# Kernel tuning notes

Measured on AMD Instinct MI355X. Metric: run time of the kernel, lower is better.

Reference implementation:

```python
import jax, jax.numpy as jnp
import numpy as np
from jax import lax

B, S, H = 4, 4096, 1024
P, D = 4096, 512
K = 3                      # conv kernel size
DILATIONS = (1, 2, 4)
TOP_K = 2
INTER = min(1024, P)       # AttentionRouter.intermediate_dim
DIV_SCALE = 0.01
LN_EPS = 1e-5


def setup_inputs() -> dict:
    key = jax.random.key(0)
    ks = jax.random.split(key, 24)
    sd = 0.02
    inp = {
        "x": jax.random.normal(ks[0], (B, S, H), jnp.float32),
        "tensor_pool": jax.random.normal(ks[1], (P, D), jnp.float32),
        # router MLP
        "w1": jax.random.normal(ks[2], (INTER, H), jnp.float32) * sd,
        "b1": jnp.zeros((INTER,), jnp.float32),
        "w2": jax.random.normal(ks[3], (P, INTER), jnp.float32) * sd,
        "b2": jnp.zeros((P,), jnp.float32),
        "temperature": jnp.float32(0.5),
        # input projection + layernorm
        "wproj": jax.random.normal(ks[4], (D, H), jnp.float32) * sd,
        "bproj": jnp.zeros((D,), jnp.float32),
        "ln_g": jnp.ones((D,), jnp.float32),
        "ln_b": jnp.zeros((D,), jnp.float32),
        # mapping linear (2D -> D)
        "wmap": jax.random.normal(ks[5], (D, 2 * D), jnp.float32) * sd,
        "bmap": jnp.zeros((D,), jnp.float32),
        # dilated convs: [n_dil, out=H, in=H, K]
        "conv_w": jax.random.normal(ks[6], (len(DILATIONS), H, H, K), jnp.float32) * sd,
        "conv_b": jnp.zeros((len(DILATIONS), H), jnp.float32),
        # conv out_proj (3H -> H)
        "wout": jax.random.normal(ks[7], (H, H * len(DILATIONS)), jnp.float32) * sd,
        "bout": jnp.zeros((H,), jnp.float32),
        # router_proj (D -> H)
        "wrp": jax.random.normal(ks[8], (H, D), jnp.float32) * sd,
        "brp": jnp.zeros((H,), jnp.float32),
        # gate_proj (H -> 1)
        "wg": jax.random.normal(ks[9], (1, H), jnp.float32) * sd,
        "bg": jnp.zeros((1,), jnp.float32),
    }
    return inp


def _layernorm(x, g, b):
    mu = jnp.mean(x, axis=-1, keepdims=True)
    var = jnp.mean(jnp.square(x - mu), axis=-1, keepdims=True)
    return (x - mu) * lax.rsqrt(var + LN_EPS) * g + b


def _forward(x, tensor_pool, w1, b1, w2, b2, temperature, wproj, bproj, ln_g, ln_b,
             wmap, bmap, conv_w, conv_b, wout, bout, wrp, brp, wg, bg):
    # ---- local branch: dilated hierarchical convolution ----
    xt = jnp.transpose(x, (0, 2, 1))  # [B,H,S]
    conv_outs = []
    for i, dil in enumerate(DILATIONS):
        pad = (K - 1) // 2 * dil
        o = lax.conv_general_dilated(
            xt, conv_w[i], window_strides=(1,), padding=[(pad, pad)],
            rhs_dilation=(dil,), dimension_numbers=("NCH", "OIH", "NCH"))
        o = o + conv_b[i][None, :, None]
        o = jax.nn.gelu(o, approximate=False)  # torch nn.GELU default (erf)
        conv_outs.append(jnp.transpose(o, (0, 2, 1)))  # [B,S,H]
    concat_out = jnp.concatenate(conv_outs, axis=-1)    # [B,S,3H]
    local_out = concat_out @ wout.T + bout               # [B,S,H]

    # ---- router (global branch) ----
    inter = jax.nn.relu(x @ w1.T + b1)                   # [B,S,INTER]
    logits = inter @ w2.T + b2                           # [B,S,P]
    temp = jnp.clip(temperature, 0.1, 5.0)
    scaled = jnp.clip(logits / temp, -10.0, 10.0)
    topk_vals, topk_idx = lax.top_k(scaled, TOP_K)       # [B,S,k]
    topk_w = jax.nn.softmax(topk_vals, axis=-1)          # [B,S,k]
    experts = tensor_pool[topk_idx]                      # [B,S,k,D] gather
    weighted_map = jnp.einsum("bsk,bskd->bsd", topk_w, experts)
    projected_x = _layernorm(x @ wproj.T + bproj, ln_g, ln_b)  # [B,S,D]
    combined = jnp.concatenate([projected_x, weighted_map], axis=-1)
    transformation = combined @ wmap.T + bmap            # [B,S,D]

    # diversity loss
    usage = jnp.zeros((P,), x.dtype).at[topk_idx.reshape(-1)].add(topk_w.reshape(-1))
    frac = usage / (usage.sum() + 1e-8)
    scale = min(1.0, (B * S * H) / (P * TOP_K))
    div_loss = jnp.mean(jnp.square(frac - 1.0 / P)) * scale * DIV_SCALE

    global_out = transformation @ wrp.T + brp            # [B,S,H]
    gate = jax.nn.sigmoid(x @ wg.T + bg)                 # [B,S,1]
    attn_out = gate * local_out + (1.0 - gate) * global_out
    return attn_out, div_loss


def reference(x, tensor_pool, w1, b1, w2, b2, temperature, wproj, bproj, ln_g, ln_b,
              wmap, bmap, conv_w, conv_b, wout, bout, wrp, brp, wg, bg):
    return _forward(x, tensor_pool, w1, b1, w2, b2, temperature, wproj, bproj,
                    ln_g, ln_b, wmap, bmap, conv_w, conv_b, wout, bout,
                    wrp, brp, wg, bg)
```

## Files before the change

### kernel.cpp

```cpp
#include <hip/hip_runtime.h>
#include <math.h>
#include <climits>

#define SQ 4096
#define HD 1024
#define PD 4096
#define DD 512
#define MR 16384
#define INTERD 1024
#define SP 4104
#define NCAND 6

typedef __attribute__((ext_vector_type(8))) short short8;
typedef __attribute__((ext_vector_type(4))) float f32x4;

__device__ __forceinline__ unsigned short f2bf(float f) {
    union { float f; unsigned u; } v; v.f = f;
    unsigned r = v.u + 0x7fff + ((v.u >> 16) & 1);
    return (unsigned short)(r >> 16);
}

__device__ __forceinline__ void gll16(const unsigned short* g, unsigned short* l) {
    __builtin_amdgcn_global_load_lds(
        (const __attribute__((address_space(1))) void*)g,
        (__attribute__((address_space(3))) void*)l, 16, 0, 0);
}

template<int AMODE, int BMODE, int EPI>
__global__ __launch_bounds__(256)
void bgemm_k(const unsigned short* __restrict__ A, int lda,
             const unsigned short* __restrict__ Bm, int ldb,
             const float* __restrict__ bias,
             float* __restrict__ Cf, unsigned short* __restrict__ Cb,
             int ldc, int coff, int K, int dil,
             const float* __restrict__ gate,
             float* __restrict__ cand_v, int* __restrict__ cand_i)
{
    __shared__ __align__(16) unsigned short As[128 * 64];
    __shared__ __align__(16) unsigned short Bs[128 * 64];
    const int tid = threadIdx.x;
    const int w = tid >> 6;
    const int ln = tid & 63;
    const int bm = blockIdx.y * 128;
    const int bn = blockIdx.x * 128;
    const int wm = (w >> 1) * 64;
    const int wn = (w & 1) * 64;

    f32x4 acc[4][4] = {};

    const int l8 = (ln & 7) * 8;
    const int rsub = w * 8 + (ln >> 3);

    for (int kt = 0; kt < K; kt += 64) {
        const int tap = kt >> 10;
        const int cin0 = kt & 1023;
#pragma unroll
        for (int q = 0; q < 4; ++q) {
            const int r = q * 32 + rsub;
            const unsigned short* asrc;
            if (AMODE == 0) {
                asrc = A + (size_t)(bm + r) * lda + kt + l8;
            } else {
                int m = bm + r;
                int b = m >> 12;
                int s = m & (SQ - 1);
                asrc = A + (size_t)(b * SP + s + 4 + (tap - 1) * dil) * 1024 + cin0 + l8;
            }
            gll16(asrc, &As[q * 2048 + w * 512]);
            const unsigned short* bsrc;
            if (BMODE == 0) {
                bsrc = Bm + (size_t)(bn + r) * ldb + kt + l8;
            } else {
                bsrc = Bm + (size_t)(tap * 1024 + bn + r) * 1024 + cin0 + l8;
            }
            gll16(bsrc, &Bs[q * 2048 + w * 512]);
        }
        __syncthreads();
#pragma unroll
        for (int ks = 0; ks < 2; ++ks) {
            const int kb = ks * 32 + (ln >> 4) * 8;
            short8 af[4], bf[4];
#pragma unroll
            for (int i = 0; i < 4; ++i)
                af[i] = *(const short8*)&As[(wm + i * 16 + (ln & 15)) * 64 + kb];
#pragma unroll
            for (int j = 0; j < 4; ++j)
                bf[j] = *(const short8*)&Bs[(wn + j * 16 + (ln & 15)) * 64 + kb];
#pragma unroll
            for (int i = 0; i < 4; ++i)
#pragma unroll
                for (int j = 0; j < 4; ++j)
                    acc[i][j] = __builtin_amdgcn_mfma_f32_16x16x32_bf16(
                        af[i], bf[j], acc[i][j], 0, 0, 0);
        }
        __syncthreads();
    }

    if constexpr (EPI == 4) {
        const int g = blockIdx.x * 2 + (w & 1);
#pragma unroll
        for (int i = 0; i < 4; ++i) {
#pragma unroll
            for (int r = 0; r < 4; ++r) {
                float v0 = -1e30f, v1 = -1e30f; int i0 = INT_MAX, i1 = INT_MAX;
#pragma unroll
                for (int j = 0; j < 4; ++j) {
                    const int col = bn + wn + j * 16 + (ln & 15);
                    float v = acc[i][j][r] + bias[col];
                    if (v > v0 || (v == v0 && col < i0)) { v1 = v0; i1 = i0; v0 = v; i0 = col; }
                    else if (v > v1 || (v == v1 && col < i1)) { v1 = v; i1 = col; }
                }
#pragma unroll
                for (int msk = 1; msk <= 8; msk <<= 1) {
                    float ov0 = __shfl_xor(v0, msk); int oi0 = __shfl_xor(i0, msk);
                    float ov1 = __shfl_xor(v1, msk); int oi1 = __shfl_xor(i1, msk);
                    if (ov0 > v0 || (ov0 == v0 && oi0 < i0)) {
                        if (v0 > ov1 || (v0 == ov1 && i0 < oi1)) { v1 = v0; i1 = i0; }
                        else { v1 = ov1; i1 = oi1; }
                        v0 = ov0; i0 = oi0;
                    } else {
                        if (ov0 > v1 || (ov0 == v1 && oi0 < i1)) { v1 = ov0; i1 = oi0; }
                    }
                }
                if ((ln & 15) == 0) {
                    const int row = bm + wm + i * 16 + (ln >> 4) * 4 + r;
                    size_t base = (size_t)row * 128 + g * 2;
                    cand_v[base] = v0; cand_v[base + 1] = v1;
                    cand_i[base] = i0; cand_i[base + 1] = i1;
                }
            }
        }
        return;
    }

#pragma unroll
    for (int i = 0; i < 4; ++i) {
        const int mrow = bm + wm + i * 16 + (ln >> 4) * 4;
#pragma unroll
        for (int j = 0; j < 4; ++j) {
            const int ncol = bn + wn + j * 16 + (ln & 15);
            const float bs = bias[ncol];
#pragma unroll
            for (int r = 0; r < 4; ++r) {
                const int m = mrow + r;
                float v = acc[i][j][r] + bs;
                if (EPI == 0) {
                    Cf[(size_t)m * ldc + coff + ncol] = v;
                } else if (EPI == 1) {
                    v = 0.5f * v * (1.0f + erff(v * 0.70710678118654752f));
                    Cb[(size_t)m * ldc + coff + ncol] = f2bf(v);
                } else if (EPI == 2) {
                    Cb[(size_t)m * ldc + coff + ncol] = f2bf(v);
                } else if (EPI == 3) {
                    float g = gate[m];
                    size_t o = (size_t)m * 1024 + ncol;
                    Cf[o] = g * v + (1.0f - g) * Cf[o];
                }
            }
        }
    }
}

__global__ __launch_bounds__(256)
void gemm_relu_k(const float* __restrict__ A, const float* __restrict__ Bm,
                 const float* __restrict__ bias,
                 float* __restrict__ C, unsigned short* __restrict__ Cb)
{
    __shared__ float As[16][68];
    __shared__ float Bs[16][68];
    const int tid = threadIdx.x;
    const int tx = tid & 15;
    const int ty = tid >> 4;
    const int bm = blockIdx.y * 64;
    const int bn = blockIdx.x * 64;

    float acc[4][4];
#pragma unroll
    for (int i = 0; i < 4; ++i)
#pragma unroll
        for (int j = 0; j < 4; ++j) acc[i][j] = 0.f;

    for (int kt = 0; kt < HD; kt += 16) {
#pragma unroll
        for (int l = 0; l < 4; ++l) {
            int idx = tid + l * 256;
            int r = idx >> 4;
            int c = idx & 15;
            As[c][r] = A[(size_t)(bm + r) * HD + (kt + c)];
            Bs[c][r] = Bm[(size_t)(bn + r) * HD + (kt + c)];
        }
        __syncthreads();
#pragma unroll
        for (int c = 0; c < 16; ++c) {
            float a[4], b[4];
#pragma unroll
            for (int i = 0; i < 4; ++i) a[i] = As[c][ty * 4 + i];
#pragma unroll
            for (int j = 0; j < 4; ++j) b[j] = Bs[c][tx * 4 + j];
#pragma unroll
            for (int i = 0; i < 4; ++i)
#pragma unroll
                for (int j = 0; j < 4; ++j)
                    acc[i][j] = fmaf(a[i], b[j], acc[i][j]);
        }
        __syncthreads();
    }
#pragma unroll
    for (int i = 0; i < 4; ++i)
#pragma unroll
        for (int j = 0; j < 4; ++j) {
            int n = bn + tx * 4 + j;
            size_t o = (size_t)(bm + ty * 4 + i) * INTERD + n;
            float v = fmaxf(acc[i][j] + bias[n], 0.f);
            C[o] = v;
            Cb[o] = f2bf(v);
        }
}

__global__ __launch_bounds__(128)
void rescore_k(const float* __restrict__ cand_v, const int* __restrict__ cand_i,
               const float* __restrict__ inter, const float* __restrict__ w2,
               const float* __restrict__ b2, const float* __restrict__ tptr,
               const float* __restrict__ pool,
               unsigned short* __restrict__ combined_b, float* __restrict__ usage)
{
    const int row = blockIdx.x;
    const int t = threadIdx.x;
    __shared__ float xs[1024];
    __shared__ float cv[128];
    __shared__ int   ci[128];
    __shared__ float rv[128];
    __shared__ int   rp[128];
    __shared__ int   ssel[NCAND];
    __shared__ float ssc[NCAND];
    __shared__ float wsh[2];
    __shared__ int   ish[2];

    const float* irow = inter + (size_t)row * INTERD;
#pragma unroll
    for (int q = 0; q < 8; ++q) xs[t + q * 128] = irow[t + q * 128];
    cv[t] = cand_v[(size_t)row * 128 + t];
    ci[t] = cand_i[(size_t)row * 128 + t];
    __syncthreads();

    for (int j = 0; j < NCAND; ++j) {
        rv[t] = cv[t]; rp[t] = t;
        __syncthreads();
        for (int o = 64; o > 0; o >>= 1) {
            if (t < o) {
                float va = rv[t], vb = rv[t + o];
                int pa = rp[t], pb = rp[t + o];
                if (vb > va || (vb == va && ci[pb] < ci[pa])) { rv[t] = vb; rp[t] = pb; }
            }
            __syncthreads();
        }
        if (t == 0) { int p = rp[0]; ssel[j] = ci[p]; cv[p] = -1e30f; }
        __syncthreads();
    }

    for (int j = 0; j < NCAND; ++j) {
        const float* wr = w2 + (size_t)ssel[j] * INTERD;
        float p = 0.f;
#pragma unroll
        for (int k = t; k < 1024; k += 128) p = fmaf(xs[k], wr[k], p);
        rv[t] = p;
        __syncthreads();
        for (int o = 64; o > 0; o >>= 1) {
            if (t < o) rv[t] += rv[t + o];
            __syncthreads();
        }
        if (t == 0) ssc[j] = rv[0] + b2[ssel[j]];
        __syncthreads();
    }

    if (t == 0) {
        float tc = fminf(fmaxf(tptr[0], 0.1f), 5.0f);
        float bv0 = -1e30f, bv1 = -1e30f; int bi0 = INT_MAX, bi1 = INT_MAX;
        for (int j = 0; j < NCAND; ++j) {
            float v = fminf(fmaxf(ssc[j] / tc, -10.f), 10.f);
            int n = ssel[j];
            if (v > bv0 || (v == bv0 && n < bi0)) { bv1 = bv0; bi1 = bi0; bv0 = v; bi0 = n; }
            else if (v > bv1 || (v == bv1 && n < bi1)) { bv1 = v; bi1 = n; }
        }
        float e1 = expf(bv1 - bv0);
        float w0 = 1.f / (1.f + e1);
        float w1 = e1 / (1.f + e1);
        atomicAdd(&usage[bi0], w0);
        atomicAdd(&usage[bi1], w1);
        wsh[0] = w0; wsh[1] = w1; ish[0] = bi0; ish[1] = bi1;
    }
    __syncthreads();
    float w0 = wsh[0], w1 = wsh[1];
    const float* p0 = pool + (size_t)ish[0] * DD;
    const float* p1 = pool + (size_t)ish[1] * DD;
    unsigned short* dst = combined_b + (size_t)row * 1024 + 512;
#pragma unroll
    for (int q = 0; q < 4; ++q) {
        int j = t + q * 128;
        dst[j] = f2bf(w0 * p0[j] + w1 * p1[j]);
    }
}

__global__ __launch_bounds__(256)
void ln_k(const float* __restrict__ projx, unsigned short* __restrict__ combined_b,
          const float* __restrict__ g, const float* __restrict__ b)
{
    int row = blockIdx.x;
    int t = threadIdx.x;
    const float* p = projx + (size_t)row * DD;
    float x0 = p[t], x1 = p[t + 256];
    __shared__ float s1[256], s2[256];
    s1[t] = x0 + x1;
    s2[t] = x0 * x0 + x1 * x1;
    __syncthreads();
    for (int o = 128; o > 0; o >>= 1) {
        if (t < o) { s1[t] += s1[t + o]; s2[t] += s2[t + o]; }
        __syncthreads();
    }
    float mu = s1[0] * (1.0f / 512.0f);
    float var = s2[0] * (1.0f / 512.0f) - mu * mu;
    float inv = rsqrtf(var + 1e-5f);
    unsigned short* dst = combined_b + (size_t)row * 1024;
    dst[t]       = f2bf((x0 - mu) * inv * g[t] + b[t]);
    dst[t + 256] = f2bf((x1 - mu) * inv * g[t + 256] + b[t + 256]);
}

__global__ __launch_bounds__(256)
void gate_k(const float* __restrict__ x, const float* __restrict__ wg,
            const float* __restrict__ bg, float* __restrict__ gate)
{
    int row = blockIdx.x;
    int t = threadIdx.x;
    const float* p = x + (size_t)row * HD;
    float s = p[t] * wg[t] + p[t + 256] * wg[t + 256]
            + p[t + 512] * wg[t + 512] + p[t + 768] * wg[t + 768];
    __shared__ float s1[256];
    s1[t] = s;
    __syncthreads();
    for (int o = 128; o > 0; o >>= 1) {
        if (t < o) s1[t] += s1[t + o];
        __syncthreads();
    }
    if (t == 0) gate[row] = 1.f / (1.f + expf(-(s1[0] + bg[0])));
}

__global__ __launch_bounds__(1024)
void divloss_k(const float* __restrict__ usage, float* __restrict__ out)
{
    int t = threadIdx.x;
    float u[4];
#pragma unroll
    for (int q = 0; q < 4; ++q) u[q] = usage[t + q * 1024];
    __shared__ float s1[1024];
    s1[t] = u[0] + u[1] + u[2] + u[3];
    __syncthreads();
    for (int o = 512; o > 0; o >>= 1) {
        if (t < o) s1[t] += s1[t + o];
        __syncthreads();
    }
    float inv = 1.0f / (s1[0] + 1e-8f);
    __syncthreads();
    float acc = 0.f;
#pragma unroll
    for (int q = 0; q < 4; ++q) {
        float d = u[q] * inv - (1.0f / 4096.0f);
        acc += d * d;
    }
    s1[t] = acc;
    __syncthreads();
    for (int o = 512; o > 0; o >>= 1) {
        if (t < o) s1[t] += s1[t + o];
        __syncthreads();
    }
    if (t == 0) out[(size_t)MR * HD] = s1[0] * (1.0f / 4096.0f) * 0.01f;
}

__global__ __launch_bounds__(256)
void xpad_k(const float* __restrict__ x, unsigned short* __restrict__ xpad)
{
    size_t idx = (size_t)blockIdx.x * 256 + threadIdx.x;
    int c = (int)(idx & 1023);
    int sp = (int)((idx >> 10) % SP);
    int b = (int)(idx / ((size_t)SP * 1024));
    float v = 0.f;
    if (sp >= 4 && sp < SQ + 4)
        v = x[((size_t)b * SQ + sp - 4) * 1024 + c];
    xpad[idx] = f2bf(v);
}

__global__ __launch_bounds__(256)
void wconv_k(const float* __restrict__ cw, unsigned short* __restrict__ wb)
{
    size_t idx = (size_t)blockIdx.x * 256 + threadIdx.x;
    int it = (int)(idx >> 20);
    int i = it / 3, tap = it % 3;
    int o = (int)((idx >> 10) & 1023);
    int in = (int)(idx & 1023);
    wb[idx] = f2bf(cw[(((size_t)(i * 1024 + o)) * 1024 + in) * 3 + tap]);
}

__global__ __launch_bounds__(256)
void cvt_k(const float* __restrict__ src, unsigned short* __restrict__ dst, int n)
{
    int idx = blockIdx.x * 256 + threadIdx.x;
    if (idx < n) dst[idx] = f2bf(src[idx]);
}

extern "C" void kernel_launch(void* const* d_in, const int* in_sizes, int n_in,
                              void* d_out, int out_size, void* d_ws, size_t ws_size,
                              hipStream_t stream)
{
    const float* x     = (const float*)d_in[0];
    const float* pool  = (const float*)d_in[1];
    const float* w1    = (const float*)d_in[2];
    const float* b1    = (const float*)d_in[3];
    const float* w2    = (const float*)d_in[4];
    const float* b2    = (const float*)d_in[5];
    const float* temp  = (const float*)d_in[6];
    const float* wproj = (const float*)d_in[7];
    const float* bproj = (const float*)d_in[8];
    const float* ln_g  = (const float*)d_in[9];
    const float* ln_b  = (const float*)d_in[10];
    const float* wmap  = (const float*)d_in[11];
    const float* bmap  = (const float*)d_in[12];
    const float* convw = (const float*)d_in[13];
    const float* convb = (const float*)d_in[14];
    const float* wout  = (const float*)d_in[15];
    const float* bout  = (const float*)d_in[16];
    const float* wrp   = (const float*)d_in[17];
    const float* brp   = (const float*)d_in[18];
    const float* wg    = (const float*)d_in[19];
    const float* bg    = (const float*)d_in[20];
    float* out = (float*)d_out;

    char* w8 = (char*)d_ws;
    float*          inter      = (float*)(w8 + 0);
    unsigned short* inter_b    = (unsigned short*)(w8 + 67108864);
    unsigned short* concat     = (unsigned short*)(w8 + 0);
    float*          projx      = (float*)(w8 + 100663296);
    unsigned short* combined_b = (unsigned short*)(w8 + 134217728);
    unsigned short* trans_b    = (unsigned short*)(w8 + 167772160);
    float*          cand_v     = (float*)(w8 + 184549376);
    int*            cand_i     = (int*)(w8 + 192937984);
    unsigned short* xpad       = (unsigned short*)(w8 + 184549376);
    unsigned short* wconvb     = (unsigned short*)(w8 + 218169344);
    unsigned short* woutb      = (unsigned short*)(w8 + 237043712);
    unsigned short* w2b        = (unsigned short*)(w8 + 237043712);
    unsigned short* wmapb      = (unsigned short*)(w8 + 243335168);
    unsigned short* wrpb       = (unsigned short*)(w8 + 244383744);
    unsigned short* wprojb     = (unsigned short*)(w8 + 245432320);
    float*          gate       = (float*)(w8 + 246480896);
    float*          usage      = (float*)(w8 + 246546432);

    hipMemsetAsync(usage, 0, PD * sizeof(float), stream);

    dim3 blk(256);
    gemm_relu_k<<<dim3(16, 256), blk, 0, stream>>>(x, w1, b1, inter, inter_b);
    cvt_k<<<dim3((PD * INTERD + 255) / 256), blk, 0, stream>>>(w2, w2b, PD * INTERD);
    bgemm_k<0, 0, 4><<<dim3(32, 128), blk, 0, stream>>>(inter_b, INTERD, w2b, INTERD,
        b2, nullptr, nullptr, 0, 0, INTERD, 0, nullptr, cand_v, cand_i);
    rescore_k<<<dim3(MR), dim3(128), 0, stream>>>(cand_v, cand_i, inter, w2, b2,
        temp, pool, combined_b, usage);

    xpad_k<<<dim3((4 * SP * 1024) / 256), blk, 0, stream>>>(x, xpad);
    wconv_k<<<dim3((9 * 1024 * 1024) / 256), blk, 0, stream>>>(convw, wconvb);
    cvt_k<<<dim3((1024 * 3072 + 255) / 256), blk, 0, stream>>>(wout, woutb, 1024 * 3072);
    cvt_k<<<dim3((512 * 1024 + 255) / 256), blk, 0, stream>>>(wmap, wmapb, 512 * 1024);
    cvt_k<<<dim3((1024 * 512 + 255) / 256), blk, 0, stream>>>(wrp, wrpb, 1024 * 512);
    cvt_k<<<dim3((512 * 1024 + 255) / 256), blk, 0, stream>>>(wproj, wprojb, 512 * 1024);

    bgemm_k<1, 0, 0><<<dim3(4, 128), blk, 0, stream>>>(xpad, 0, wprojb, HD, bproj,
        projx, nullptr, DD, 0, HD, 0, nullptr, nullptr, nullptr);
    ln_k<<<dim3(MR), dim3(256), 0, stream>>>(projx, combined_b, ln_g, ln_b);
    bgemm_k<0, 0, 2><<<dim3(4, 128), blk, 0, stream>>>(combined_b, 1024, wmapb, 1024,
        bmap, nullptr, trans_b, DD, 0, 1024, 0, nullptr, nullptr, nullptr);
    bgemm_k<0, 0, 0><<<dim3(8, 128), blk, 0, stream>>>(trans_b, DD, wrpb, DD, brp,
        out, nullptr, HD, 0, DD, 0, nullptr, nullptr, nullptr);
    gate_k<<<dim3(MR), dim3(256), 0, stream>>>(x, wg, bg, gate);
    divloss_k<<<dim3(1), dim3(1024), 0, stream>>>(usage, out);

    const int dils[3] = {1, 2, 4};
    for (int i = 0; i < 3; ++i) {
        bgemm_k<1, 1, 1><<<dim3(8, 128), blk, 0, stream>>>(
            xpad, 0, wconvb + (size_t)i * 3 * 1024 * 1024, 0,
            convb + (size_t)i * HD,
            nullptr, concat, 3072, i * 1024, 3072, dils[i], nullptr, nullptr, nullptr);
    }
    bgemm_k<0, 0, 3><<<dim3(8, 128), blk, 0, stream>>>(concat, 3072, woutb, 3072,
        bout, out, nullptr, HD, 0, 3072, 0, gate, nullptr, nullptr);
}
```

Before: 1.973 ms.

## Enlarge fp32 router GEMM tiles, shuffle-based rescore, tanh GELU approximation

The fp32 router GEMM now uses 128x128 tiles with 8x8 per-thread register blocking, float4 global and LDS loads, and vectorized fp32/bf16 stores. This raises arithmetic intensity over the old 64x64, 4x4 version. The rescore kernel replaces its LDS tree reductions and repeated barriers with wave shuffles, and keeps the intermediate row in registers. The erf GELU in the conv epilogue becomes a tanh approximation using __expf, which changes numerics slightly.

```diff
diff --git a/kernel.cpp b/kernel.cpp
--- a/kernel.cpp
+++ b/kernel.cpp
@@ -24,6 +24,13 @@
     __builtin_amdgcn_global_load_lds(
         (const __attribute__((address_space(1))) void*)g,
         (__attribute__((address_space(3))) void*)l, 16, 0, 0);
+}
+
+__device__ __forceinline__ float gelu_f(float v) {
+    float u = v * (0.7978845608028654f + 0.03567740813636141f * v * v);
+    float e = __expf(2.0f * u);
+    float th = 1.0f - 2.0f / (e + 1.0f);
+    return 0.5f * v * (1.0f + th);
 }
 
 template<int AMODE, int BMODE, int EPI>
@@ -147,8 +154,7 @@
                 if (EPI == 0) {
                     Cf[(size_t)m * ldc + coff + ncol] = v;
                 } else if (EPI == 1) {
-                    v = 0.5f * v * (1.0f + erff(v * 0.70710678118654752f));
-                    Cb[(size_t)m * ldc + coff + ncol] = f2bf(v);
+                    Cb[(size_t)m * ldc + coff + ncol] = f2bf(gelu_f(v));
                 } else if (EPI == 2) {
                     Cb[(size_t)m * ldc + coff + ncol] = f2bf(v);
                 } else if (EPI == 3) {
@@ -162,59 +168,74 @@
 }
 
 __global__ __launch_bounds__(256)
-void gemm_relu_k(const float* __restrict__ A, const float* __restrict__ Bm,
-                 const float* __restrict__ bias,
-                 float* __restrict__ C, unsigned short* __restrict__ Cb)
-{
-    __shared__ float As[16][68];
-    __shared__ float Bs[16][68];
+void gemm_relu2_k(const float* __restrict__ A, const float* __restrict__ Bm,
+                  const float* __restrict__ bias,
+                  float* __restrict__ C, unsigned short* __restrict__ Cb)
+{
+    __shared__ __align__(16) float As[16 * 132];
+    __shared__ __align__(16) float Bs[16 * 132];
     const int tid = threadIdx.x;
     const int tx = tid & 15;
     const int ty = tid >> 4;
-    const int bm = blockIdx.y * 64;
-    const int bn = blockIdx.x * 64;
-
-    float acc[4][4];
-#pragma unroll
-    for (int i = 0; i < 4; ++i)
-#pragma unroll
-        for (int j = 0; j < 4; ++j) acc[i][j] = 0.f;
+    const int bm = blockIdx.y * 128;
+    const int bn = blockIdx.x * 128;
+
+    float acc[8][8] = {};
 
     for (int kt = 0; kt < HD; kt += 16) {
 #pragma unroll
-        for (int l = 0; l < 4; ++l) {
+        for (int l = 0; l < 2; ++l) {
             int idx = tid + l * 256;
-            int r = idx >> 4;
-            int c = idx & 15;
-            As[c][r] = A[(size_t)(bm + r) * HD + (kt + c)];
-            Bs[c][r] = Bm[(size_t)(bn + r) * HD + (kt + c)];
+            int m = idx >> 2;
+            int c4 = (idx & 3) * 4;
+            float4 va = *(const float4*)&A[(size_t)(bm + m) * HD + kt + c4];
+            As[(c4 + 0) * 132 + m] = va.x;
+            As[(c4 + 1) * 132 + m] = va.y;
+            As[(c4 + 2) * 132 + m] = va.z;
+            As[(c4 + 3) * 132 + m] = va.w;
+            float4 vb = *(const float4*)&Bm[(size_t)(bn + m) * HD + kt + c4];
+            Bs[(c4 + 0) * 132 + m] = vb.x;
+            Bs[(c4 + 1) * 132 + m] = vb.y;
+            Bs[(c4 + 2) * 132 + m] = vb.z;
+            Bs[(c4 + 3) * 132 + m] = vb.w;
         }
         __syncthreads();
 #pragma unroll
         for (int c = 0; c < 16; ++c) {
-            float a[4], b[4];
-#pragma unroll
-            for (int i = 0; i < 4; ++i) a[i] = As[c][ty * 4 + i];
-#pragma unroll
-            for (int j = 0; j < 4; ++j) b[j] = Bs[c][tx * 4 + j];
-#pragma unroll
-            for (int i = 0; i < 4; ++i)
-#pragma unroll
-                for (int j = 0; j < 4; ++j)
+            float4 a0 = *(const float4*)&As[c * 132 + ty * 8];
+            float4 a1 = *(const float4*)&As[c * 132 + ty * 8 + 4];
+            float4 b0 = *(const float4*)&Bs[c * 132 + tx * 8];
+            float4 b1 = *(const float4*)&Bs[c * 132 + tx * 8 + 4];
+            float a[8] = {a0.x, a0.y, a0.z, a0.w, a1.x, a1.y, a1.z, a1.w};
+            float b[8] = {b0.x, b0.y, b0.z, b0.w, b1.x, b1.y, b1.z, b1.w};
+#pragma unroll
+            for (int i = 0; i < 8; ++i)
+#pragma unroll
+                for (int j = 0; j < 8; ++j)
                     acc[i][j] = fmaf(a[i], b[j], acc[i][j]);
         }
         __syncthreads();
     }
-#pragma unroll
-    for (int i = 0; i < 4; ++i)
-#pragma unroll
-        for (int j = 0; j < 4; ++j) {
-            int n = bn + tx * 4 + j;
-            size_t o = (size_t)(bm + ty * 4 + i) * INTERD + n;
-            float v = fmaxf(acc[i][j] + bias[n], 0.f);
-            C[o] = v;
-            Cb[o] = f2bf(v);
-        }
+
+    float bs[8];
+#pragma unroll
+    for (int j = 0; j < 8; ++j) bs[j] = bias[bn + tx * 8 + j];
+#pragma unroll
+    for (int i = 0; i < 8; ++i) {
+        const int m = bm + ty * 8 + i;
+        float v[8];
+#pragma unroll
+        for (int j = 0; j < 8; ++j) v[j] = fmaxf(acc[i][j] + bs[j], 0.f);
+        float* cp = C + (size_t)m * INTERD + bn + tx * 8;
+        *(float4*)cp = make_float4(v[0], v[1], v[2], v[3]);
+        *(float4*)(cp + 4) = make_float4(v[4], v[5], v[6], v[7]);
+        unsigned u[4];
+#pragma unroll
+        for (int j = 0; j < 4; ++j)
+            u[j] = (unsigned)f2bf(v[2 * j]) | ((unsigned)f2bf(v[2 * j + 1]) << 16);
+        *(uint4*)(Cb + (size_t)m * INTERD + bn + tx * 8) =
+            make_uint4(u[0], u[1], u[2], u[3]);
+    }
 }
 
 __global__ __launch_bounds__(128)
@@ -226,59 +247,71 @@
 {
     const int row = blockIdx.x;
     const int t = threadIdx.x;
-    __shared__ float xs[1024];
-    __shared__ float cv[128];
-    __shared__ int   ci[128];
-    __shared__ float rv[128];
-    __shared__ int   rp[128];
+    const int lane = t & 63;
+    const int wv = t >> 6;
     __shared__ int   ssel[NCAND];
-    __shared__ float ssc[NCAND];
+    __shared__ float pw[2][NCAND];
     __shared__ float wsh[2];
     __shared__ int   ish[2];
 
+    float xr[8];
     const float* irow = inter + (size_t)row * INTERD;
 #pragma unroll
-    for (int q = 0; q < 8; ++q) xs[t + q * 128] = irow[t + q * 128];
-    cv[t] = cand_v[(size_t)row * 128 + t];
-    ci[t] = cand_i[(size_t)row * 128 + t];
-    __syncthreads();
-
+    for (int q = 0; q < 8; ++q) xr[q] = irow[t + q * 128];
+
+    if (wv == 0) {
+        float v0 = cand_v[(size_t)row * 128 + lane];
+        float v1 = cand_v[(size_t)row * 128 + 64 + lane];
+        int   i0 = cand_i[(size_t)row * 128 + lane];
+        int   i1 = cand_i[(size_t)row * 128 + 64 + lane];
+        if (v1 > v0 || (v1 == v0 && i1 < i0)) {
+            float tv = v0; v0 = v1; v1 = tv;
+            int ti = i0; i0 = i1; i1 = ti;
+        }
+        for (int j = 0; j < NCAND; ++j) {
+            float bv = v0; int bi = i0;
+#pragma unroll
+            for (int m = 32; m >= 1; m >>= 1) {
+                float ov = __shfl_xor(bv, m);
+                int oi = __shfl_xor(bi, m);
+                if (ov > bv || (ov == bv && oi < bi)) { bv = ov; bi = oi; }
+            }
+            if (lane == 0) ssel[j] = bi;
+            if (i0 == bi) { v0 = v1; i0 = i1; v1 = -1e30f; i1 = INT_MAX; }
+        }
+    }
+    __syncthreads();
+
+    int sel[NCAND];
+#pragma unroll
+    for (int j = 0; j < NCAND; ++j) sel[j] = ssel[j];
+    float p[NCAND];
+#pragma unroll
     for (int j = 0; j < NCAND; ++j) {
-        rv[t] = cv[t]; rp[t] = t;
-        __syncthreads();
-        for (int o = 64; o > 0; o >>= 1) {
-            if (t < o) {
-                float va = rv[t], vb = rv[t + o];
-                int pa = rp[t], pb = rp[t + o];
-                if (vb > va || (vb == va && ci[pb] < ci[pa])) { rv[t] = vb; rp[t] = pb; }
-            }
-            __syncthreads();
-        }
-        if (t == 0) { int p = rp[0]; ssel[j] = ci[p]; cv[p] = -1e30f; }
-        __syncthreads();
-    }
-
+        const float* wr = w2 + (size_t)sel[j] * INTERD + t;
+        float pj = 0.f;
+#pragma unroll
+        for (int q = 0; q < 8; ++q) pj = fmaf(xr[q], wr[q * 128], pj);
+        p[j] = pj;
+    }
+#pragma unroll
     for (int j = 0; j < NCAND; ++j) {
-        const float* wr = w2 + (size_t)ssel[j] * INTERD;
-        float p = 0.f;
-#pragma unroll
-        for (int k = t; k < 1024; k += 128) p = fmaf(xs[k], wr[k], p);
-        rv[t] = p;
-        __syncthreads();
-        for (int o = 64; o > 0; o >>= 1) {
-            if (t < o) rv[t] += rv[t + o];
-            __syncthreads();
-        }
-        if (t == 0) ssc[j] = rv[0] + b2[ssel[j]];
-        __syncthreads();
-    }
+#pragma unroll
+        for (int m = 32; m >= 1; m >>= 1) p[j] += __shfl_xor(p[j], m);
+    }
+    if (lane == 0) {
+#pragma unroll
+        for (int j = 0; j < NCAND; ++j) pw[wv][j] = p[j];
+    }
+    __syncthreads();
 
     if (t == 0) {
         float tc = fminf(fmaxf(tptr[0], 0.1f), 5.0f);
         float bv0 = -1e30f, bv1 = -1e30f; int bi0 = INT_MAX, bi1 = INT_MAX;
         for (int j = 0; j < NCAND; ++j) {
-            float v = fminf(fmaxf(ssc[j] / tc, -10.f), 10.f);
-            int n = ssel[j];
+            float logit = pw[0][j] + pw[1][j] + b2[sel[j]];
+            float v = fminf(fmaxf(logit / tc, -10.f), 10.f);
+            int n = sel[j];
             if (v > bv0 || (v == bv0 && n < bi0)) { bv1 = bv0; bi1 = bi0; bv0 = v; bi0 = n; }
             else if (v > bv1 || (v == bv1 && n < bi1)) { bv1 = v; bi1 = n; }
         }
@@ -455,7 +488,7 @@
     hipMemsetAsync(usage, 0, PD * sizeof(float), stream);
 
     dim3 blk(256);
-    gemm_relu_k<<<dim3(16, 256), blk, 0, stream>>>(x, w1, b1, inter, inter_b);
+    gemm_relu2_k<<<dim3(8, 128), blk, 0, stream>>>(x, w1, b1, inter, inter_b);
     cvt_k<<<dim3((PD * INTERD + 255) / 256), blk, 0, stream>>>(w2, w2b, PD * INTERD);
     bgemm_k<0, 0, 4><<<dim3(32, 128), blk, 0, stream>>>(inter_b, INTERD, w2b, INTERD,
         b2, nullptr, nullptr, 0, 0, INTERD, 0, nullptr, cand_v, cand_i);
```

After: 1.872 ms. -5.1%, faster.
